# Optimization experiments

Hardware: AMD Instinct MI355X
Metric: run time of the kernel (lower is better)

The kernel has to match this reference:

```python
import jax, jax.numpy as jnp
import numpy as np

N_NODES = 100000
N_EDGES = 1600000
IN_DIM = 128
OUT_DIM = 128


def setup_inputs() -> dict:
    key = jax.random.key(0)
    k1, k2, k3, k4, k5 = jax.random.split(key, 5)
    x = jax.random.normal(k1, (N_NODES, IN_DIM), dtype=jnp.float32)
    edge_index = jax.random.randint(k2, (2, N_EDGES), 0, N_NODES, dtype=jnp.int64)
    s = 1.0 / np.sqrt(IN_DIM)
    # PyG SAGEConv params: lin_l (neighbor branch, with bias), lin_r (root branch, no bias)
    W_l = jax.random.uniform(k3, (OUT_DIM, IN_DIM), jnp.float32, -s, s)
    b_l = jax.random.uniform(k4, (OUT_DIM,), jnp.float32, -s, s)
    W_r = jax.random.uniform(k5, (OUT_DIM, IN_DIM), jnp.float32, -s, s)
    return {"x": x, "edge_index": edge_index, "W_l": W_l, "b_l": b_l, "W_r": W_r}


def reference(x, edge_index, W_l, b_l, W_r):
    src = edge_index[0]  # message source j
    dst = edge_index[1]  # aggregation target i
    # mean aggregation of neighbor features at each target node
    msg_sum = jax.ops.segment_sum(x[src], dst, num_segments=N_NODES)  # [N, in]
    deg = jax.ops.segment_sum(jnp.ones((N_EDGES,), x.dtype), dst, num_segments=N_NODES)
    agg = msg_sum / jnp.maximum(deg, 1.0)[:, None]
    # out = lin_l(agg) + lin_r(x)
    out = agg @ W_l.T + b_l + x @ W_r.T  # [N, out]
    # L2 normalize (F.normalize, p=2, dim=-1, eps=1e-12)
    norm = jnp.sqrt(jnp.sum(out * out, axis=-1, keepdims=True))
    out = out / jnp.maximum(norm, 1e-12)
    return out
```

## Files before the change

### kernel.cpp

```cpp
#include <hip/hip_runtime.h>
#include <hip/hip_fp16.h>
#include <stdint.h>

#define NN 100000
#define D 128
#define W0 128
#define NB ((NN + W0 - 1) / W0)
#define C1 4096
#define CAP 4096
#define OVF_CAP 65536

typedef _Float16 f16x8 __attribute__((ext_vector_type(8)));
typedef float f32x4 __attribute__((ext_vector_type(4)));

static const size_t O_FLAG   = 0;
static const size_t O_BCNT   = 256;
static const size_t O_BSTART = O_BCNT + 4096;
static const size_t O_BCUR   = O_BSTART + 4096;
static const size_t O_WTL    = O_BCUR + 4096;
static const size_t O_WTR    = O_WTL + (size_t)D * D * 4;
static const size_t O_OFFS   = O_WTR + (size_t)D * D * 4;
static const size_t O_DEG    = O_OFFS + (size_t)(NN + 64) * 4;
static const size_t O_RECS   = O_DEG + (size_t)NN * 4;
static const size_t O_OVF    = O_RECS + (size_t)NB * CAP * 4;
static const size_t O_XH     = O_OVF + (size_t)OVF_CAP * 8;

__device__ __forceinline__ int edge_at(const int* ei, long long pos, int is64) {
    return is64 ? ei[2 * pos] : ei[pos];
}

__device__ __forceinline__ void detect_is64(const int* __restrict__ ei, long long E,
                                            int t, int* s_is64) {
    if (t < 64) {
        int bad = 0;
        if (t < E)      bad |= (ei[2 * t + 1] != 0);
        if (t + 64 < E) bad |= (ei[2 * (t + 64) + 1] != 0);
        unsigned long long m = __ballot(bad);
        if (t == 0) *s_is64 = (m == 0ull) ? 1 : 0;
    }
}

__global__ __launch_bounds__(256) void k_build(
        const float* __restrict__ x, const int* __restrict__ ei,
        const float* __restrict__ Wl, const float* __restrict__ Wr,
        __half* __restrict__ xh, __half* __restrict__ Bp,
        int* __restrict__ bcur, int* __restrict__ ovf_cnt,
        unsigned long long* __restrict__ ovf,
        unsigned int* __restrict__ recs, long long E)
{
    __shared__ int cnt[NB];
    __shared__ int rbase[NB];
    __shared__ int s_is64;
    int t = threadIdx.x, b = blockIdx.x;
    detect_is64(ei, E, t, &s_is64);
    for (int i = t; i < NB; i += 256) cnt[i] = 0;
    __syncthreads();
    int is64 = s_is64;

    int idx = b * 256 + t;
    if (idx < 32768) {
        int j  = idx & 7;
        int l  = (idx >> 3) & 63;
        int tt = (idx >> 9) & 7;
        int s  = idx >> 12;
        int col = tt * 16 + (l & 15);
        int k   = s * 32 + (l >> 4) * 8 + j;
        float v = (k < 128) ? Wl[col * 128 + k] : Wr[col * 128 + (k - 128)];
        Bp[idx] = __float2half_rn(v);
    }
    const long long n4 = (long long)NN * D / 4;
    for (long long i = (long long)b * 256 + t; i < n4; i += (long long)gridDim.x * 256) {
        float4 v = ((const float4*)x)[i];
        ((__half2*)xh)[2 * i]     = __floats2half2_rn(v.x, v.y);
        ((__half2*)xh)[2 * i + 1] = __floats2half2_rn(v.z, v.w);
    }
    long long base = (long long)b * C1;
    for (int j = t; j < C1; j += 256) {
        long long e = base + j;
        if (e < E) atomicAdd(&cnt[edge_at(ei, E + e, is64) >> 7], 1);
    }
    __syncthreads();
    for (int i = t; i < NB; i += 256) {
        int c = cnt[i];
        rbase[i] = c ? atomicAdd(&bcur[i], c) : 0;
        cnt[i] = 0;
    }
    __syncthreads();
    for (int j = t; j < C1; j += 256) {
        long long e = base + j;
        if (e < E) {
            int s = edge_at(ei, e, is64);
            int d = edge_at(ei, E + e, is64);
            int bu = d >> 7;
            unsigned rec = (unsigned)s | ((unsigned)(d & (W0 - 1)) << 20);
            int pos = rbase[bu] + atomicAdd(&cnt[bu], 1);
            if (pos < CAP) recs[(long long)bu * CAP + pos] = rec;
            else {
                int op = atomicAdd(ovf_cnt, 1);
                if (op < OVF_CAP) ovf[op] = ((unsigned long long)bu << 32) | rec;
            }
        }
    }
}

__global__ __launch_bounds__(512) void k_p2agg_g(
        const unsigned int* __restrict__ recs,
        const int* __restrict__ bcur, const int* __restrict__ ovf_cnt,
        const unsigned long long* __restrict__ ovf,
        const __half* __restrict__ xh, const __half* __restrict__ Bp,
        const float* __restrict__ bl, float* __restrict__ out, int N)
{
    __shared__ int cnt[W0];
    __shared__ int off[W0];
    __shared__ int sl[CAP];
    __shared__ __half aw[8][16][136];
    __shared__ int s_oc;
    int t = threadIdx.x, b = blockIdx.x;
    long long e0g = (long long)b * CAP;
    int ne = bcur[b];
    if (ne > CAP) ne = CAP;
    if (t == 0) s_oc = min(*ovf_cnt, OVF_CAP);

    if (t < W0) cnt[t] = 0;
    __syncthreads();
    for (int e = t; e < ne; e += 512)
        atomicAdd(&cnt[recs[e0g + e] >> 20], 1);
    __syncthreads();
    if (t < W0) off[t] = cnt[t];
    __syncthreads();
    for (int d = 1; d < W0; d <<= 1) {
        int v = 0;
        if (t < W0 && t >= d) v = off[t - d];
        __syncthreads();
        if (t < W0) off[t] += v;
        __syncthreads();
    }
    if (t < W0) cnt[t] = (t > 0) ? off[t - 1] : 0;
    __syncthreads();
    for (int e = t; e < ne; e += 512) {
        unsigned r = recs[e0g + e];
        int pos = atomicAdd(&cnt[r >> 20], 1);
        sl[pos] = (int)(r & 0xFFFFFu);
    }
    __syncthreads();

    int lane = t & 63;
    int wid  = t >> 6;
    int oc   = s_oc;
    const __half2* x2 = (const __half2*)xh;

    for (int i = 0; i < 16; ++i) {
        int n = wid * 16 + i;
        int node = b * W0 + n;
        if (node >= N) break;
        int s0 = (n > 0) ? off[n - 1] : 0;
        int s1 = off[n];
        float ax = 0.f, ay = 0.f;
        int e = s0;
        for (; e + 8 <= s1; e += 8) {
            int ss[8];
#pragma unroll
            for (int u = 0; u < 8; ++u) ss[u] = sl[e + u];
            __half2 h[8];
#pragma unroll
            for (int u = 0; u < 8; ++u) h[u] = x2[(long long)ss[u] * 64 + lane];
#pragma unroll
            for (int u = 0; u < 8; ++u) {
                float2 v = __half22float2(h[u]);
                ax += v.x; ay += v.y;
            }
        }
        for (; e + 2 <= s1; e += 2) {
            int sa = sl[e], sb = sl[e + 1];
            float2 v0 = __half22float2(x2[(long long)sa * 64 + lane]);
            float2 v1 = __half22float2(x2[(long long)sb * 64 + lane]);
            ax += v0.x + v1.x;
            ay += v0.y + v1.y;
        }
        if (e < s1) {
            float2 v = __half22float2(x2[(long long)sl[e] * 64 + lane]);
            ax += v.x; ay += v.y;
        }
        int extra = 0;
        for (int k = 0; k < oc; ++k) {
            unsigned long long v = ovf[k];
            if ((int)(v >> 32) == b) {
                unsigned rec = (unsigned)v;
                if ((int)(rec >> 20) == n) {
                    float2 w = __half22float2(x2[(long long)(rec & 0xFFFFFu) * 64 + lane]);
                    ax += w.x; ay += w.y; ++extra;
                }
            }
        }
        float inv = 1.0f / fmaxf((float)(s1 - s0 + extra), 1.0f);
        *(__half2*)&aw[wid][i][2 * lane] = __floats2half2_rn(ax * inv, ay * inv);
    }

    f32x4 acc[8];
#pragma unroll
    for (int c = 0; c < 8; ++c) acc[c] = (f32x4){0.f, 0.f, 0.f, 0.f};

    int rn = b * W0 + wid * 16 + (lane & 15);
    long long rx = (rn < N) ? rn : (N - 1);
    int koff = (lane >> 4) * 8;
#pragma unroll
    for (int s = 0; s < 8; ++s) {
        f16x8 a;
        if (s < 4) a = *(const f16x8*)&aw[wid][lane & 15][s * 32 + koff];
        else       a = *(const f16x8*)(xh + rx * 128 + (s & 3) * 32 + koff);
        const __half* bp = Bp + ((s * 8) * 64 + lane) * 8;
#pragma unroll
        for (int tt = 0; tt < 8; ++tt) {
            f16x8 bf = *(const f16x8*)(bp + tt * 512);
            acc[tt] = __builtin_amdgcn_mfma_f32_16x16x32_f16(a, bf, acc[tt], 0, 0, 0);
        }
    }

    float bias[8];
#pragma unroll
    for (int tt = 0; tt < 8; ++tt) bias[tt] = bl[tt * 16 + (lane & 15)];

#pragma unroll
    for (int r = 0; r < 4; ++r) {
        int n = (lane >> 4) * 4 + r;
        int node = b * W0 + wid * 16 + n;
        float v[8];
        float ss = 0.f;
#pragma unroll
        for (int tt = 0; tt < 8; ++tt) {
            v[tt] = acc[tt][r] + bias[tt];
            ss = fmaf(v[tt], v[tt], ss);
        }
        ss += __shfl_xor(ss, 1, 64);
        ss += __shfl_xor(ss, 2, 64);
        ss += __shfl_xor(ss, 4, 64);
        ss += __shfl_xor(ss, 8, 64);
        float scale = 1.0f / fmaxf(sqrtf(ss), 1e-12f);
        if (node < N) {
            float* op = out + (long long)node * D + (lane & 15);
#pragma unroll
            for (int tt = 0; tt < 8; ++tt)
                op[tt * 16] = v[tt] * scale;
        }
    }
}

__global__ void k_detect(const int* __restrict__ ei, int* flag, long long E) {
    int l = threadIdx.x;
    int bad = 0;
    if (l < E)       bad |= (ei[2 * l + 1] != 0);
    if (l + 64 < E)  bad |= (ei[2 * (l + 64) + 1] != 0);
    unsigned long long m = __ballot(bad);
    if (l == 0) *flag = (m == 0ull) ? 1 : 0;
}

__global__ void k_transpose(const float* __restrict__ Wl, const float* __restrict__ Wr,
                            float* __restrict__ WtL, float* __restrict__ WtR) {
    int t = blockIdx.x * 256 + threadIdx.x;
    if (t < D * D) {
        int o = t >> 7, k = t & 127;
        WtL[k * D + o] = Wl[t];
        WtR[k * D + o] = Wr[t];
    }
}

__global__ __launch_bounds__(256) void k_p1count(const int* __restrict__ ei,
                                                 const int* __restrict__ flag,
                                                 int* __restrict__ bcount, long long E) {
    __shared__ int cnt[NB];
    for (int i = threadIdx.x; i < NB; i += 256) cnt[i] = 0;
    __syncthreads();
    int is64 = *flag;
    long long base = (long long)blockIdx.x * C1;
    for (int j = threadIdx.x; j < C1; j += 256) {
        long long e = base + j;
        if (e < E) atomicAdd(&cnt[edge_at(ei, E + e, is64) >> 7], 1);
    }
    __syncthreads();
    for (int i = threadIdx.x; i < NB; i += 256) {
        int c = cnt[i];
        if (c) atomicAdd(&bcount[i], c);
    }
}

__global__ __launch_bounds__(1024) void k_bscan(const int* __restrict__ bcount,
                                                int* __restrict__ bstart,
                                                int* __restrict__ bcur,
                                                int* __restrict__ offs) {
    __shared__ int sh[1024];
    int t = threadIdx.x;
    sh[t] = (t < NB) ? bcount[t] : 0;
    __syncthreads();
    for (int d = 1; d < 1024; d <<= 1) {
        int v = (t >= d) ? sh[t - d] : 0;
        __syncthreads();
        sh[t] += v;
        __syncthreads();
    }
    if (t < NB) {
        int ex = (t > 0) ? sh[t - 1] : 0;
        bstart[t] = ex;
        bcur[t] = ex;
    }
    if (t == NB - 1) {
        bstart[NB] = sh[NB - 1];
        offs[NN] = sh[NB - 1];
    }
}

__global__ __launch_bounds__(256) void k_p1scatter(const int* __restrict__ ei,
                                                   const int* __restrict__ flag,
                                                   int* __restrict__ bcur,
                                                   unsigned int* __restrict__ recs,
                                                   long long E) {
    __shared__ int cnt[NB];
    __shared__ int rbase[NB];
    for (int i = threadIdx.x; i < NB; i += 256) cnt[i] = 0;
    __syncthreads();
    int is64 = *flag;
    long long base = (long long)blockIdx.x * C1;
    for (int j = threadIdx.x; j < C1; j += 256) {
        long long e = base + j;
        if (e < E) atomicAdd(&cnt[edge_at(ei, E + e, is64) >> 7], 1);
    }
    __syncthreads();
    for (int i = threadIdx.x; i < NB; i += 256) {
        int c = cnt[i];
        rbase[i] = c ? atomicAdd(&bcur[i], c) : 0;
    }
    __syncthreads();
    for (int i = threadIdx.x; i < NB; i += 256) cnt[i] = 0;
    __syncthreads();
    for (int j = threadIdx.x; j < C1; j += 256) {
        long long e = base + j;
        if (e < E) {
            int s = edge_at(ei, e, is64);
            int d = edge_at(ei, E + e, is64);
            int bu = d >> 7;
            int pos = rbase[bu] + atomicAdd(&cnt[bu], 1);
            recs[pos] = (unsigned)s | ((unsigned)(d & (W0 - 1)) << 20);
        }
    }
}

__global__ __launch_bounds__(256) void k_p2(const unsigned int* __restrict__ recs,
                                            const int* __restrict__ bstart,
                                            int* __restrict__ offs,
                                            int* __restrict__ srcs, int N) {
    __shared__ int cnt[W0];
    __shared__ int off[W0];
    int t = threadIdx.x;
    int bu = blockIdx.x;
    int e0 = bstart[bu], e1 = bstart[bu + 1];
    if (t < W0) cnt[t] = 0;
    __syncthreads();
    for (int e = e0 + t; e < e1; e += 256)
        atomicAdd(&cnt[recs[e] >> 20], 1);
    __syncthreads();
    if (t < W0) off[t] = cnt[t];
    __syncthreads();
    for (int d = 1; d < W0; d <<= 1) {
        int v = 0;
        if (t < W0 && t >= d) v = off[t - d];
        __syncthreads();
        if (t < W0) off[t] += v;
        __syncthreads();
    }
    if (t < W0) {
        int ex = (t > 0) ? off[t - 1] : 0;
        int node = bu * W0 + t;
        if (node < N) offs[node] = e0 + ex;
        cnt[t] = e0 + ex;
    }
    __syncthreads();
    for (int e = e0 + t; e < e1; e += 256) {
        unsigned r = recs[e];
        int pos = atomicAdd(&cnt[r >> 20], 1);
        srcs[pos] = (int)(r & 0xFFFFFu);
    }
}

__global__ __launch_bounds__(256) void k_agg(const float* __restrict__ x,
                                             const int* __restrict__ offs,
                                             const int* __restrict__ srcs,
                                             float* agg, int N) {
    int lane = threadIdx.x & 63;
    int wid = __builtin_amdgcn_readfirstlane(threadIdx.x >> 6);
    int node = blockIdx.x * 4 + wid;
    if (node >= N) return;
    int e0 = offs[node], e1 = offs[node + 1];
    const float2* x2 = (const float2*)x;
    float ax = 0.f, ay = 0.f;
    int e = e0;
    for (; e + 4 <= e1; e += 4) {
        int s0 = srcs[e], s1 = srcs[e + 1], s2 = srcs[e + 2], s3 = srcs[e + 3];
        float2 v0 = x2[(long long)s0 * 64 + lane];
        float2 v1 = x2[(long long)s1 * 64 + lane];
        float2 v2 = x2[(long long)s2 * 64 + lane];
        float2 v3 = x2[(long long)s3 * 64 + lane];
        ax += v0.x + v1.x + v2.x + v3.x;
        ay += v0.y + v1.y + v2.y + v3.y;
    }
    for (; e < e1; ++e) {
        int s = srcs[e];
        float2 v = x2[(long long)s * 64 + lane];
        ax += v.x; ay += v.y;
    }
    float inv = 1.0f / fmaxf((float)(e1 - e0), 1.0f);
    float2 o; o.x = ax * inv; o.y = ay * inv;
    ((float2*)agg)[(long long)node * 64 + lane] = o;
}

__global__ __launch_bounds__(256) void k_scatterB(const float* __restrict__ x,
                                                  const int* __restrict__ ei,
                                                  const int* __restrict__ flag,
                                                  float* out, float* deg, long long E) {
    int lane = threadIdx.x & 63;
    long long e = (long long)blockIdx.x * 4 + (threadIdx.x >> 6);
    if (e >= E) return;
    int is64 = *flag;
    int s = edge_at(ei, e, is64);
    int d = edge_at(ei, E + e, is64);
    atomicAdd(&out[(long long)d * D + lane], x[(long long)s * D + lane]);
    atomicAdd(&out[(long long)d * D + 64 + lane], x[(long long)s * D + 64 + lane]);
    if (lane == 0) atomicAdd(&deg[d], 1.0f);
}

__global__ void k_meanB(float* out, const float* __restrict__ deg) {
    long long i = (long long)blockIdx.x * 256 + threadIdx.x;
    if (i >= (long long)NN * D) return;
    out[i] *= 1.0f / fmaxf(deg[i >> 7], 1.0f);
}

__global__ __launch_bounds__(256) void k_gemm(const float* __restrict__ x,
                                              const float* agg,
                                              const float* __restrict__ WtL,
                                              const float* __restrict__ WtR,
                                              const float* __restrict__ bl,
                                              float* out, int N) {
    __shared__ float Bs[64 * D];
    int t = threadIdx.x;
    int tx = t & 15;
    int ty = t >> 4;
    int row0 = blockIdx.x * 64 + ty * 4;
    int c0a = tx * 4;
    int c0b = 64 + tx * 4;

    float acc[4][8];
    float4 b0 = *(const float4*)(bl + c0a);
    float4 b1 = *(const float4*)(bl + c0b);
#pragma unroll
    for (int r = 0; r < 4; ++r) {
        acc[r][0] = b0.x; acc[r][1] = b0.y; acc[r][2] = b0.z; acc[r][3] = b0.w;
        acc[r][4] = b1.x; acc[r][5] = b1.y; acc[r][6] = b1.z; acc[r][7] = b1.w;
    }

    long long rws[4];
#pragma unroll
    for (int r = 0; r < 4; ++r) {
        int rr = row0 + r;
        rws[r] = (rr < N) ? (long long)rr : (long long)(N - 1);
    }

    for (int phase = 0; phase < 2; ++phase) {
        const float* A = phase ? x : agg;
        const float* W = phase ? WtR : WtL;
        const float4* Ar0 = (const float4*)(A + rws[0] * D);
        const float4* Ar1 = (const float4*)(A + rws[1] * D);
        const float4* Ar2 = (const float4*)(A + rws[2] * D);
        const float4* Ar3 = (const float4*)(A + rws[3] * D);

        for (int half = 0; half < 2; ++half) {
            if (phase | half) __syncthreads();
#pragma unroll
            for (int i = 0; i < 8; ++i) {
                int idx = t + i * 256;
                ((float4*)Bs)[idx] = ((const float4*)(W + half * 64 * D))[idx];
            }
            __syncthreads();

#pragma unroll 2
            for (int k4 = 0; k4 < 16; ++k4) {
                int ak4 = half * 16 + k4;
                float4 av[4];
                av[0] = Ar0[ak4]; av[1] = Ar1[ak4]; av[2] = Ar2[ak4]; av[3] = Ar3[ak4];
#pragma unroll
                for (int kk = 0; kk < 4; ++kk) {
                    int k = k4 * 4 + kk;
                    float4 w0 = *(const float4*)&Bs[k * D + c0a];
                    float4 w1 = *(const float4*)&Bs[k * D + c0b];
#pragma unroll
                    for (int r = 0; r < 4; ++r) {
                        float a = (kk == 0) ? av[r].x : (kk == 1) ? av[r].y
                                 : (kk == 2) ? av[r].z : av[r].w;
                        acc[r][0] = fmaf(a, w0.x, acc[r][0]);
                        acc[r][1] = fmaf(a, w0.y, acc[r][1]);
                        acc[r][2] = fmaf(a, w0.z, acc[r][2]);
                        acc[r][3] = fmaf(a, w0.w, acc[r][3]);
                        acc[r][4] = fmaf(a, w1.x, acc[r][4]);
                        acc[r][5] = fmaf(a, w1.y, acc[r][5]);
                        acc[r][6] = fmaf(a, w1.z, acc[r][6]);
                        acc[r][7] = fmaf(a, w1.w, acc[r][7]);
                    }
                }
            }
        }
    }

#pragma unroll
    for (int r = 0; r < 4; ++r) {
        float s = 0.f;
#pragma unroll
        for (int j = 0; j < 8; ++j) s = fmaf(acc[r][j], acc[r][j], s);
        s += __shfl_xor(s, 1, 64);
        s += __shfl_xor(s, 2, 64);
        s += __shfl_xor(s, 4, 64);
        s += __shfl_xor(s, 8, 64);
        float scale = 1.0f / fmaxf(sqrtf(s), 1e-12f);
        int rr = row0 + r;
        if (rr < N) {
            float4 v0, v1;
            v0.x = acc[r][0] * scale; v0.y = acc[r][1] * scale;
            v0.z = acc[r][2] * scale; v0.w = acc[r][3] * scale;
            v1.x = acc[r][4] * scale; v1.y = acc[r][5] * scale;
            v1.z = acc[r][6] * scale; v1.w = acc[r][7] * scale;
            float* op = out + (long long)rr * D;
            *(float4*)(op + c0a) = v0;
            *(float4*)(op + c0b) = v1;
        }
    }
}

extern "C" void kernel_launch(void* const* d_in, const int* in_sizes, int n_in,
                              void* d_out, int out_size, void* d_ws, size_t ws_size,
                              hipStream_t stream) {
    const float* x  = (const float*)d_in[0];
    const int*   ei = (const int*)d_in[1];
    const float* Wl = (const float*)d_in[2];
    const float* bl = (const float*)d_in[3];
    const float* Wr = (const float*)d_in[4];
    float* out = (float*)d_out;
    const long long E = (long long)in_sizes[1] / 2;

    char* ws = (char*)d_ws;
    int*      flag   = (int*)(ws + O_FLAG);
    int*      bcount = (int*)(ws + O_BCNT);
    int*      bstart = (int*)(ws + O_BSTART);
    int*      bcur   = (int*)(ws + O_BCUR);
    int*      ovfc   = (int*)(ws + O_BCUR + 3200);
    float*    WtL    = (float*)(ws + O_WTL);
    float*    WtR    = (float*)(ws + O_WTR);
    __half*   Bph    = (__half*)(ws + O_WTL);
    int*      offs   = (int*)(ws + O_OFFS);
    float*    deg    = (float*)(ws + O_DEG);
    unsigned* recs   = (unsigned*)(ws + O_RECS);
    int*      srcs   = (int*)(ws + O_RECS + (size_t)E * 4);
    unsigned long long* ovf = (unsigned long long*)(ws + O_OVF);
    __half*   xh     = (__half*)(ws + O_XH);

    int pb = (int)((E + C1 - 1) / C1);
    size_t planA_bytes = O_RECS + (size_t)E * 8;
    size_t fast_bytes  = O_XH + (size_t)NN * D * 2;
    bool planA = ws_size >= planA_bytes;
    bool useF  = (ws_size >= fast_bytes) && (E <= (long long)NB * CAP);

    if (useF) {
        hipMemsetAsync(ws + O_BCUR, 0, 4096, stream);
        k_build<<<pb, 256, 0, stream>>>(x, ei, Wl, Wr, xh, Bph, bcur, ovfc, ovf, recs, E);
        k_p2agg_g<<<NB, 512, 0, stream>>>(recs, bcur, ovfc, ovf, xh, Bph, bl, out, NN);
        return;
    }

    k_detect<<<1, 64, 0, stream>>>(ei, flag, E);
    k_transpose<<<(D * D + 255) / 256, 256, 0, stream>>>(Wl, Wr, WtL, WtR);

    if (planA) {
        hipMemsetAsync(ws + O_BCNT, 0, (size_t)NB * 4, stream);
        k_p1count<<<pb, 256, 0, stream>>>(ei, flag, bcount, E);
        k_bscan<<<1, 1024, 0, stream>>>(bcount, bstart, bcur, offs);
        k_p1scatter<<<pb, 256, 0, stream>>>(ei, flag, bcur, recs, E);
        k_p2<<<NB, 256, 0, stream>>>(recs, bstart, offs, srcs, NN);
        k_agg<<<(NN + 3) / 4, 256, 0, stream>>>(x, offs, srcs, out, NN);
    } else {
        hipMemsetAsync(out, 0, (size_t)NN * D * 4, stream);
        hipMemsetAsync(ws + O_DEG, 0, (size_t)NN * 4, stream);
        k_scatterB<<<(int)((E + 3) / 4), 256, 0, stream>>>(x, ei, flag, out, deg, E);
        k_meanB<<<(int)(((long long)NN * D + 255) / 256), 256, 0, stream>>>(out, deg);
    }
    k_gemm<<<(NN + 63) / 64, 256, 0, stream>>>(x, out, WtL, WtR, bl, out, NN);
}
```

Before: 246.4 us.

## Replace bucket sort with per-node fixed-capacity adjacency slots and fused agg-GEMM

```diff
diff --git a/kernel.cpp b/kernel.cpp
--- a/kernel.cpp
+++ b/kernel.cpp
@@ -8,6 +8,7 @@
 #define NB ((NN + W0 - 1) / W0)
 #define C1 4096
 #define CAP 4096
+#define NCAP 64
 #define OVF_CAP 65536
 
 typedef _Float16 f16x8 __attribute__((ext_vector_type(8)));
@@ -22,8 +23,6 @@
 static const size_t O_OFFS   = O_WTR + (size_t)D * D * 4;
 static const size_t O_DEG    = O_OFFS + (size_t)(NN + 64) * 4;
 static const size_t O_RECS   = O_DEG + (size_t)NN * 4;
-static const size_t O_OVF    = O_RECS + (size_t)NB * CAP * 4;
-static const size_t O_XH     = O_OVF + (size_t)OVF_CAP * 8;
 
 __device__ __forceinline__ int edge_at(const int* ei, long long pos, int is64) {
     return is64 ? ei[2 * pos] : ei[pos];
@@ -37,6 +36,160 @@
         if (t + 64 < E) bad |= (ei[2 * (t + 64) + 1] != 0);
         unsigned long long m = __ballot(bad);
         if (t == 0) *s_is64 = (m == 0ull) ? 1 : 0;
+    }
+}
+
+__global__ __launch_bounds__(256) void k_build2(
+        const float* __restrict__ x, const int* __restrict__ ei,
+        const float* __restrict__ Wl, const float* __restrict__ Wr,
+        __half* __restrict__ xh, __half* __restrict__ Bp,
+        int* __restrict__ ncur, int* __restrict__ ovfc,
+        unsigned long long* __restrict__ ovf,
+        int* __restrict__ nrec, long long E)
+{
+    __shared__ int s_is64;
+    int t = threadIdx.x, b = blockIdx.x;
+    detect_is64(ei, E, t, &s_is64);
+    __syncthreads();
+    int is64 = s_is64;
+
+    int idx = b * 256 + t;
+    if (idx < 32768) {
+        int j  = idx & 7;
+        int l  = (idx >> 3) & 63;
+        int tt = (idx >> 9) & 7;
+        int s  = idx >> 12;
+        int col = tt * 16 + (l & 15);
+        int k   = s * 32 + (l >> 4) * 8 + j;
+        float v = (k < 128) ? Wl[col * 128 + k] : Wr[col * 128 + (k - 128)];
+        Bp[idx] = __float2half_rn(v);
+    }
+    const long long n4 = (long long)NN * D / 4;
+    for (long long i = (long long)b * 256 + t; i < n4; i += (long long)gridDim.x * 256) {
+        float4 v = ((const float4*)x)[i];
+        ((__half2*)xh)[2 * i]     = __floats2half2_rn(v.x, v.y);
+        ((__half2*)xh)[2 * i + 1] = __floats2half2_rn(v.z, v.w);
+    }
+    long long base = (long long)b * C1;
+    for (int j = t; j < C1; j += 256) {
+        long long e = base + j;
+        if (e < E) {
+            int s = edge_at(ei, e, is64);
+            int d = edge_at(ei, E + e, is64);
+            int pos = atomicAdd(&ncur[d], 1);
+            if (pos < NCAP) nrec[(long long)d * NCAP + pos] = s;
+            else {
+                int op = atomicAdd(ovfc, 1);
+                if (op < OVF_CAP) ovf[op] = ((unsigned long long)d << 32) | (unsigned)s;
+            }
+        }
+    }
+}
+
+__global__ __launch_bounds__(256) void k_aggemm(
+        const int* __restrict__ nrec, const int* __restrict__ ncur,
+        const int* __restrict__ ovfc, const unsigned long long* __restrict__ ovf,
+        const __half* __restrict__ xh, const __half* __restrict__ Bp,
+        const float* __restrict__ bl, float* __restrict__ out, int N)
+{
+    __shared__ __half aw[4][16][132];
+    int t = threadIdx.x, b = blockIdx.x;
+    int lane = t & 63;
+    int wid  = t >> 6;
+    int oc = *ovfc;
+    if (oc > OVF_CAP) oc = OVF_CAP;
+    const __half2* x2 = (const __half2*)xh;
+
+    for (int i = 0; i < 16; ++i) {
+        int node = b * 64 + wid * 16 + i;
+        if (node >= N) break;
+        int deg = ncur[node];
+        int cnt = (deg < NCAP) ? deg : NCAP;
+        const int* sp = nrec + (long long)node * NCAP;
+        float ax = 0.f, ay = 0.f;
+        int e = 0;
+        for (; e + 8 <= cnt; e += 8) {
+            int ss[8];
+#pragma unroll
+            for (int u = 0; u < 8; ++u) ss[u] = sp[e + u];
+            __half2 h[8];
+#pragma unroll
+            for (int u = 0; u < 8; ++u) h[u] = x2[(long long)ss[u] * 64 + lane];
+#pragma unroll
+            for (int u = 0; u < 8; ++u) {
+                float2 v = __half22float2(h[u]);
+                ax += v.x; ay += v.y;
+            }
+        }
+        for (; e + 2 <= cnt; e += 2) {
+            int sa = sp[e], sb = sp[e + 1];
+            float2 v0 = __half22float2(x2[(long long)sa * 64 + lane]);
+            float2 v1 = __half22float2(x2[(long long)sb * 64 + lane]);
+            ax += v0.x + v1.x;
+            ay += v0.y + v1.y;
+        }
+        if (e < cnt) {
+            float2 v = __half22float2(x2[(long long)sp[e] * 64 + lane]);
+            ax += v.x; ay += v.y;
+        }
+        if (deg > NCAP && oc > 0) {
+            for (int k = 0; k < oc; ++k) {
+                unsigned long long v = ovf[k];
+                if ((int)(v >> 32) == node) {
+                    float2 w = __half22float2(x2[(long long)(unsigned)v * 64 + lane]);
+                    ax += w.x; ay += w.y;
+                }
+            }
+        }
+        float inv = 1.0f / fmaxf((float)deg, 1.0f);
+        *(__half2*)&aw[wid][i][2 * lane] = __floats2half2_rn(ax * inv, ay * inv);
+    }
+
+    f32x4 acc[8];
+#pragma unroll
+    for (int c = 0; c < 8; ++c) acc[c] = (f32x4){0.f, 0.f, 0.f, 0.f};
+
+    int rn = b * 64 + wid * 16 + (lane & 15);
+    long long rx = (rn < N) ? rn : (N - 1);
+    int koff = (lane >> 4) * 8;
+#pragma unroll
+    for (int s = 0; s < 8; ++s) {
+        f16x8 a;
+        if (s < 4) a = *(const f16x8*)&aw[wid][lane & 15][s * 32 + koff];
+        else       a = *(const f16x8*)(xh + rx * 128 + (s & 3) * 32 + koff);
+        const __half* bp = Bp + ((s * 8) * 64 + lane) * 8;
+#pragma unroll
+        for (int tt = 0; tt < 8; ++tt) {
+            f16x8 bf = *(const f16x8*)(bp + tt * 512);
+            acc[tt] = __builtin_amdgcn_mfma_f32_16x16x32_f16(a, bf, acc[tt], 0, 0, 0);
+        }
+    }
+
+    float bias[8];
+#pragma unroll
+    for (int tt = 0; tt < 8; ++tt) bias[tt] = bl[tt * 16 + (lane & 15)];
+
+#pragma unroll
+    for (int r = 0; r < 4; ++r) {
+        int node = b * 64 + wid * 16 + (lane >> 4) * 4 + r;
+        float v[8];
+        float ss = 0.f;
+#pragma unroll
+        for (int tt = 0; tt < 8; ++tt) {
+            v[tt] = acc[tt][r] + bias[tt];
+            ss = fmaf(v[tt], v[tt], ss);
+        }
+        ss += __shfl_xor(ss, 1, 64);
+        ss += __shfl_xor(ss, 2, 64);
+        ss += __shfl_xor(ss, 4, 64);
+        ss += __shfl_xor(ss, 8, 64);
+        float scale = 1.0f / fmaxf(sqrtf(ss), 1e-12f);
+        if (node < N) {
+            float* op = out + (long long)node * D + (lane & 15);
+#pragma unroll
+            for (int tt = 0; tt < 8; ++tt)
+                op[tt * 16] = v[tt] * scale;
+        }
     }
 }
 
@@ -222,8 +375,7 @@
 
 #pragma unroll
     for (int r = 0; r < 4; ++r) {
-        int n = (lane >> 4) * 4 + r;
-        int node = b * W0 + wid * 16 + n;
+        int node = b * W0 + wid * 16 + (lane >> 4) * 4 + r;
         float v[8];
         float ss = 0.f;
 #pragma unroll
@@ -547,7 +699,7 @@
     int*      bcount = (int*)(ws + O_BCNT);
     int*      bstart = (int*)(ws + O_BSTART);
     int*      bcur   = (int*)(ws + O_BCUR);
-    int*      ovfc   = (int*)(ws + O_BCUR + 3200);
+    int*      ovfcM  = (int*)(ws + O_BCUR + 3200);
     float*    WtL    = (float*)(ws + O_WTL);
     float*    WtR    = (float*)(ws + O_WTR);
     __half*   Bph    = (__half*)(ws + O_WTL);
@@ -555,22 +707,45 @@
     float*    deg    = (float*)(ws + O_DEG);
     unsigned* recs   = (unsigned*)(ws + O_RECS);
     int*      srcs   = (int*)(ws + O_RECS + (size_t)E * 4);
-    unsigned long long* ovf = (unsigned long long*)(ws + O_OVF);
-    __half*   xh     = (__half*)(ws + O_XH);
 
     int pb = (int)((E + C1 - 1) / C1);
-    size_t planA_bytes = O_RECS + (size_t)E * 8;
-    size_t fast_bytes  = O_XH + (size_t)NN * D * 2;
-    bool planA = ws_size >= planA_bytes;
-    bool useF  = (ws_size >= fast_bytes) && (E <= (long long)NB * CAP);
-
-    if (useF) {
-        hipMemsetAsync(ws + O_BCUR, 0, 4096, stream);
-        k_build<<<pb, 256, 0, stream>>>(x, ei, Wl, Wr, xh, Bph, bcur, ovfc, ovf, recs, E);
-        k_p2agg_g<<<NB, 512, 0, stream>>>(recs, bcur, ovfc, ovf, xh, Bph, bl, out, NN);
-        return;
-    }
-
+
+    {
+        int*  ncur = (int*)(ws + O_OFFS);
+        int*  ovfc = ncur + NN;
+        int*  nrec = (int*)(ws + O_RECS);
+        const size_t O_OVF_N = O_RECS + (size_t)NN * NCAP * 4;
+        unsigned long long* ovfN = (unsigned long long*)(ws + O_OVF_N);
+        const size_t O_XH_N = O_OVF_N + (size_t)OVF_CAP * 8;
+        __half* xh = (__half*)(ws + O_XH_N);
+        size_t need = O_XH_N + (size_t)NN * D * 2;
+        if (ws_size >= need) {
+            hipMemsetAsync(ncur, 0, (size_t)(NN + 64) * 4, stream);
+            k_build2<<<pb, 256, 0, stream>>>(x, ei, Wl, Wr, xh, Bph,
+                                             ncur, ovfc, ovfN, nrec, E);
+            k_aggemm<<<(NN + 63) / 64, 256, 0, stream>>>(nrec, ncur, ovfc, ovfN,
+                                                         xh, Bph, bl, out, NN);
+            return;
+        }
+    }
+
+    {
+        const size_t O_OVF = O_RECS + (size_t)NB * CAP * 4;
+        unsigned long long* ovf = (unsigned long long*)(ws + O_OVF);
+        const size_t O_XH = O_OVF + (size_t)OVF_CAP * 8;
+        __half* xh = (__half*)(ws + O_XH);
+        size_t need = O_XH + (size_t)NN * D * 2;
+        if (ws_size >= need && E <= (long long)NB * CAP) {
+            hipMemsetAsync(ws + O_BCUR, 0, 4096, stream);
+            k_build<<<pb, 256, 0, stream>>>(x, ei, Wl, Wr, xh, Bph,
+                                            bcur, ovfcM, ovf, recs, E);
+            k_p2agg_g<<<NB, 512, 0, stream>>>(recs, bcur, ovfcM, ovf,
+                                              xh, Bph, bl, out, NN);
+            return;
+        }
+    }
+
+    bool planA = ws_size >= O_RECS + (size_t)E * 8;
     k_detect<<<1, 64, 0, stream>>>(ei, flag, E);
     k_transpose<<<(D * D + 255) / 256, 256, 0, stream>>>(Wl, Wr, WtL, WtR);
 
```

New measurement: 353.6 us. 1.44x slower.

## Split aggregation from GEMM and cache edge pairs in shared memory during build

Applied to the files above, without the earlier changes.

```diff
diff --git a/kernel.cpp b/kernel.cpp
--- a/kernel.cpp
+++ b/kernel.cpp
@@ -24,6 +24,7 @@
 static const size_t O_RECS   = O_DEG + (size_t)NN * 4;
 static const size_t O_OVF    = O_RECS + (size_t)NB * CAP * 4;
 static const size_t O_XH     = O_OVF + (size_t)OVF_CAP * 8;
+static const size_t O_AGGH   = O_XH + (size_t)NN * D * 2;
 
 __device__ __forceinline__ int edge_at(const int* ei, long long pos, int is64) {
     return is64 ? ei[2 * pos] : ei[pos];
@@ -48,6 +49,7 @@
         unsigned long long* __restrict__ ovf,
         unsigned int* __restrict__ recs, long long E)
 {
+    __shared__ int2 ed[C1];
     __shared__ int cnt[NB];
     __shared__ int rbase[NB];
     __shared__ int s_is64;
@@ -75,9 +77,13 @@
         ((__half2*)xh)[2 * i + 1] = __floats2half2_rn(v.z, v.w);
     }
     long long base = (long long)b * C1;
-    for (int j = t; j < C1; j += 256) {
+    int m = (int)(((base + C1) <= E) ? C1 : (E > base ? E - base : 0));
+    for (int j = t; j < m; j += 256) {
         long long e = base + j;
-        if (e < E) atomicAdd(&cnt[edge_at(ei, E + e, is64) >> 7], 1);
+        int s = edge_at(ei, e, is64);
+        int d = edge_at(ei, E + e, is64);
+        ed[j] = make_int2(s, d);
+        atomicAdd(&cnt[d >> 7], 1);
     }
     __syncthreads();
     for (int i = t; i < NB; i += 256) {
@@ -86,34 +92,28 @@
         cnt[i] = 0;
     }
     __syncthreads();
-    for (int j = t; j < C1; j += 256) {
-        long long e = base + j;
-        if (e < E) {
-            int s = edge_at(ei, e, is64);
-            int d = edge_at(ei, E + e, is64);
-            int bu = d >> 7;
-            unsigned rec = (unsigned)s | ((unsigned)(d & (W0 - 1)) << 20);
-            int pos = rbase[bu] + atomicAdd(&cnt[bu], 1);
-            if (pos < CAP) recs[(long long)bu * CAP + pos] = rec;
-            else {
-                int op = atomicAdd(ovf_cnt, 1);
-                if (op < OVF_CAP) ovf[op] = ((unsigned long long)bu << 32) | rec;
-            }
-        }
-    }
-}
-
-__global__ __launch_bounds__(512) void k_p2agg_g(
+    for (int j = t; j < m; j += 256) {
+        int s = ed[j].x, d = ed[j].y;
+        int bu = d >> 7;
+        unsigned rec = (unsigned)s | ((unsigned)(d & (W0 - 1)) << 20);
+        int pos = rbase[bu] + atomicAdd(&cnt[bu], 1);
+        if (pos < CAP) recs[(long long)bu * CAP + pos] = rec;
+        else {
+            int op = atomicAdd(ovf_cnt, 1);
+            if (op < OVF_CAP) ovf[op] = ((unsigned long long)bu << 32) | rec;
+        }
+    }
+}
+
+__global__ __launch_bounds__(512) void k_p2agg(
         const unsigned int* __restrict__ recs,
         const int* __restrict__ bcur, const int* __restrict__ ovf_cnt,
         const unsigned long long* __restrict__ ovf,
-        const __half* __restrict__ xh, const __half* __restrict__ Bp,
-        const float* __restrict__ bl, float* __restrict__ out, int N)
+        const __half* __restrict__ xh, __half* __restrict__ aggh, int N)
 {
     __shared__ int cnt[W0];
     __shared__ int off[W0];
     __shared__ int sl[CAP];
-    __shared__ __half aw[8][16][136];
     __shared__ int s_oc;
     int t = threadIdx.x, b = blockIdx.x;
     long long e0g = (long long)b * CAP;
@@ -193,26 +193,53 @@
             }
         }
         float inv = 1.0f / fmaxf((float)(s1 - s0 + extra), 1.0f);
-        *(__half2*)&aw[wid][i][2 * lane] = __floats2half2_rn(ax * inv, ay * inv);
-    }
-
-    f32x4 acc[8];
-#pragma unroll
-    for (int c = 0; c < 8; ++c) acc[c] = (f32x4){0.f, 0.f, 0.f, 0.f};
-
-    int rn = b * W0 + wid * 16 + (lane & 15);
-    long long rx = (rn < N) ? rn : (N - 1);
+        ((__half2*)aggh)[(long long)node * 64 + lane] =
+            __floats2half2_rn(ax * inv, ay * inv);
+    }
+}
+
+__global__ __launch_bounds__(256) void k_gemm_m(const __half* __restrict__ aggh,
+                                                const __half* __restrict__ xh,
+                                                const __half* __restrict__ Bp,
+                                                const float* __restrict__ bl,
+                                                float* __restrict__ out, int N) {
+    __shared__ __half Bs[32768];
+    int t = threadIdx.x;
+#pragma unroll
+    for (int i = 0; i < 16; ++i) {
+        int idx = t + i * 256;
+        ((float4*)Bs)[idx] = ((const float4*)Bp)[idx];
+    }
+    int lane = t & 63;
+    int wid  = t >> 6;
+    int row0 = blockIdx.x * 128 + wid * 32;
+    int rA = row0 + (lane & 15);
+    int rB = rA + 16;
+    long long ra = (rA < N) ? rA : (N - 1);
+    long long rb = (rB < N) ? rB : (N - 1);
     int koff = (lane >> 4) * 8;
+
+    f32x4 acc[2][8];
+#pragma unroll
+    for (int r = 0; r < 2; ++r)
+#pragma unroll
+        for (int c = 0; c < 8; ++c)
+            acc[r][c] = (f32x4){0.f, 0.f, 0.f, 0.f};
+
+    __syncthreads();
+
 #pragma unroll
     for (int s = 0; s < 8; ++s) {
-        f16x8 a;
-        if (s < 4) a = *(const f16x8*)&aw[wid][lane & 15][s * 32 + koff];
-        else       a = *(const f16x8*)(xh + rx * 128 + (s & 3) * 32 + koff);
-        const __half* bp = Bp + ((s * 8) * 64 + lane) * 8;
+        const __half* Ap = (s < 4) ? aggh : xh;
+        int kb = (s & 3) * 32 + koff;
+        f16x8 a0 = *(const f16x8*)(Ap + ra * 128 + kb);
+        f16x8 a1 = *(const f16x8*)(Ap + rb * 128 + kb);
+        const __half* bs = Bs + s * 4096 + lane * 8;
 #pragma unroll
         for (int tt = 0; tt < 8; ++tt) {
-            f16x8 bf = *(const f16x8*)(bp + tt * 512);
-            acc[tt] = __builtin_amdgcn_mfma_f32_16x16x32_f16(a, bf, acc[tt], 0, 0, 0);
+            f16x8 bf = *(const f16x8*)(bs + tt * 512);
+            acc[0][tt] = __builtin_amdgcn_mfma_f32_16x16x32_f16(a0, bf, acc[0][tt], 0, 0, 0);
+            acc[1][tt] = __builtin_amdgcn_mfma_f32_16x16x32_f16(a1, bf, acc[1][tt], 0, 0, 0);
         }
     }
 
@@ -221,26 +248,28 @@
     for (int tt = 0; tt < 8; ++tt) bias[tt] = bl[tt * 16 + (lane & 15)];
 
 #pragma unroll
-    for (int r = 0; r < 4; ++r) {
-        int n = (lane >> 4) * 4 + r;
-        int node = b * W0 + wid * 16 + n;
-        float v[8];
-        float ss = 0.f;
-#pragma unroll
-        for (int tt = 0; tt < 8; ++tt) {
-            v[tt] = acc[tt][r] + bias[tt];
-            ss = fmaf(v[tt], v[tt], ss);
-        }
-        ss += __shfl_xor(ss, 1, 64);
-        ss += __shfl_xor(ss, 2, 64);
-        ss += __shfl_xor(ss, 4, 64);
-        ss += __shfl_xor(ss, 8, 64);
-        float scale = 1.0f / fmaxf(sqrtf(ss), 1e-12f);
-        if (node < N) {
-            float* op = out + (long long)node * D + (lane & 15);
-#pragma unroll
-            for (int tt = 0; tt < 8; ++tt)
-                op[tt * 16] = v[tt] * scale;
+    for (int rt = 0; rt < 2; ++rt) {
+#pragma unroll
+        for (int r = 0; r < 4; ++r) {
+            int row = row0 + rt * 16 + (lane >> 4) * 4 + r;
+            float v[8];
+            float ss = 0.f;
+#pragma unroll
+            for (int tt = 0; tt < 8; ++tt) {
+                v[tt] = acc[rt][tt][r] + bias[tt];
+                ss = fmaf(v[tt], v[tt], ss);
+            }
+            ss += __shfl_xor(ss, 1, 64);
+            ss += __shfl_xor(ss, 2, 64);
+            ss += __shfl_xor(ss, 4, 64);
+            ss += __shfl_xor(ss, 8, 64);
+            float scale = 1.0f / fmaxf(sqrtf(ss), 1e-12f);
+            if (row < N) {
+                float* op = out + (long long)row * D + (lane & 15);
+#pragma unroll
+                for (int tt = 0; tt < 8; ++tt)
+                    op[tt * 16] = v[tt] * scale;
+            }
         }
     }
 }
@@ -557,20 +586,21 @@
     int*      srcs   = (int*)(ws + O_RECS + (size_t)E * 4);
     unsigned long long* ovf = (unsigned long long*)(ws + O_OVF);
     __half*   xh     = (__half*)(ws + O_XH);
+    __half*   aggh   = (__half*)(ws + O_AGGH);
 
     int pb = (int)((E + C1 - 1) / C1);
-    size_t planA_bytes = O_RECS + (size_t)E * 8;
-    size_t fast_bytes  = O_XH + (size_t)NN * D * 2;
-    bool planA = ws_size >= planA_bytes;
-    bool useF  = (ws_size >= fast_bytes) && (E <= (long long)NB * CAP);
+    size_t fast_bytes = O_AGGH + (size_t)NN * D * 2;
+    bool useF = (ws_size >= fast_bytes) && (E <= (long long)NB * CAP);
 
     if (useF) {
         hipMemsetAsync(ws + O_BCUR, 0, 4096, stream);
         k_build<<<pb, 256, 0, stream>>>(x, ei, Wl, Wr, xh, Bph, bcur, ovfc, ovf, recs, E);
-        k_p2agg_g<<<NB, 512, 0, stream>>>(recs, bcur, ovfc, ovf, xh, Bph, bl, out, NN);
+        k_p2agg<<<NB, 512, 0, stream>>>(recs, bcur, ovfc, ovf, xh, aggh, NN);
+        k_gemm_m<<<(NN + 127) / 128, 256, 0, stream>>>(aggh, xh, Bph, bl, out, NN);
         return;
     }
 
+    bool planA = ws_size >= O_RECS + (size_t)E * 8;
     k_detect<<<1, 64, 0, stream>>>(ei, flag, E);
     k_transpose<<<(D * D + 255) / 256, 256, 0, stream>>>(Wl, Wr, WtL, WtR);
 
```

Result: faster. 220.6 us (-10.5%).
